# Kernel tuning notes

Hardware: AMD Instinct MI355X
Metric: run time of the kernel (lower is better)

## Reference

```python
import jax, jax.numpy as jnp
import numpy as np

D_MODEL = 256
D_INNER = 512          # expand * d_model
HEADDIM = 64
NHEADS = D_INNER // HEADDIM   # 8
NGROUPS = 1
D_STATE = 64
D_IN_PROJ = 2 * D_INNER + 2 * NGROUPS * D_STATE + NHEADS   # 1160
CONV_DIM = D_INNER + 2 * NGROUPS * D_STATE                  # 640
LN_EPS = 1e-5


def setup_inputs() -> dict:
    key = jax.random.key(0)
    ks = jax.random.split(key, 16)
    s = 0.02
    # dt_bias init as in torch code
    dt = jnp.exp(jax.random.uniform(ks[10], (NHEADS,)) * (np.log(0.1) - np.log(0.001)) + np.log(0.001))
    dt = jnp.clip(dt, 1e-4)
    dt_bias = dt + jnp.log(-jnp.expm1(-dt))
    A_log = jnp.log(jax.random.uniform(ks[11], (NHEADS,), minval=1.0, maxval=16.0))
    return {
        "u": jax.random.normal(ks[0], (4, 8192, D_MODEL), dtype=jnp.float32),
        "H": 64,
        "W": 128,
        "W_in": jax.random.normal(ks[1], (D_IN_PROJ, D_MODEL), dtype=jnp.float32) * s,
        "W_stereo": jax.random.normal(ks[2], (D_IN_PROJ, D_INNER), dtype=jnp.float32) * s,
        "conv_l_w": jax.random.normal(ks[3], (CONV_DIM, 1, 3, 3), dtype=jnp.float32) * 0.1,
        "conv_l_b": jax.random.normal(ks[4], (CONV_DIM,), dtype=jnp.float32) * 0.01,
        "conv_r_w": jax.random.normal(ks[5], (CONV_DIM, 1, 3, 3), dtype=jnp.float32) * 0.1,
        "conv_r_b": jax.random.normal(ks[6], (CONV_DIM,), dtype=jnp.float32) * 0.01,
        "conv_w": jax.random.normal(ks[7], (CONV_DIM, 1, 3, 3), dtype=jnp.float32) * 0.1,
        "conv_b": jax.random.normal(ks[8], (CONV_DIM,), dtype=jnp.float32) * 0.01,
        "dt_bias": dt_bias,
        "A_log": A_log,
        "D_l": jnp.ones((NHEADS,), dtype=jnp.float32),
        "D_r": jnp.ones((NHEADS,), dtype=jnp.float32),
        "D": jnp.ones((NHEADS,), dtype=jnp.float32),
        "ln_g": jnp.ones((D_INNER,), dtype=jnp.float32),
        "ln_b": jnp.zeros((D_INNER,), dtype=jnp.float32),
        "W_out": jax.random.normal(ks[9], (D_MODEL, D_INNER), dtype=jnp.float32) * s,
    }


def _dwconv(x, w, b):
    # x: (B, C, H, W); depthwise 3x3 conv, SAME padding ((d_conv-1)//2 = 1)
    y = jax.lax.conv_general_dilated(
        x, w, window_strides=(1, 1), padding='SAME',
        dimension_numbers=('NCHW', 'OIHW', 'NCHW'),
        feature_group_count=CONV_DIM)
    return y + b[None, :, None, None]


def _layernorm(x, g, b):
    mu = x.mean(-1, keepdims=True)
    var = x.var(-1, keepdims=True)
    return (x - mu) / jnp.sqrt(var + LN_EPS) * g + b


def _lin_attn(x, dt, A, Bm, Cm, Dp):
    # x: (b, l, d_inner), dt: (b, l, h), Bm/Cm: (b, l, d_state); ngroups == 1
    b, l, _ = x.shape
    xh = x.reshape(b, l, NHEADS, HEADDIM)              # V: (b, l, h, p)
    dA = -(dt[..., None] * A[None, None, :, None])     # ssd_positve_dA -> -dt*A, (b,l,h,1)
    KV = jnp.einsum('bls,blhp->bhsp', Bm, xh * dA)     # K^T @ V_scaled
    y = jnp.einsum('bls,bhsp->blhp', Cm, KV)           # Q @ KV
    y = y + xh * Dp[None, None, :, None]               # skip D
    return y.reshape(b, l, D_INNER)


def reference(u, H, W, W_in, W_stereo, conv_l_w, conv_l_b, conv_r_w, conv_r_b,
              conv_w, conv_b, dt_bias, A_log, D_l, D_r, D, ln_g, ln_b, W_out):
    batch, seqlen, _ = u.shape
    half = batch // 2
    silu = jax.nn.silu
    A = -jnp.exp(A_log)

    zxbcdt = u @ W_in.T                                             # (b, l, 1160)
    z, xBC, dt = jnp.split(zxbcdt, [D_INNER, D_INNER + CONV_DIM], axis=-1)
    dt = jax.nn.softplus(dt + dt_bias)                              # (b, l, h)

    xBC = xBC.reshape(batch, H, W, CONV_DIM).transpose(0, 3, 1, 2)  # NCHW
    xBC1 = silu(_dwconv(xBC[:half], conv_l_w, conv_l_b)).transpose(0, 2, 3, 1).reshape(half, H * W, CONV_DIM)
    xBC2 = silu(_dwconv(xBC[half:], conv_r_w, conv_r_b)).transpose(0, 2, 3, 1).reshape(half, H * W, CONV_DIM)

    x1, B1, C1 = jnp.split(xBC1, [D_INNER, D_INNER + NGROUPS * D_STATE], axis=-1)
    x2, B2, C2 = jnp.split(xBC2, [D_INNER, D_INNER + NGROUPS * D_STATE], axis=-1)
    dt1, dt2 = dt[:half], dt[half:]

    y1 = _layernorm(_lin_attn(x1, dt1, A, B1, C1, D_l), ln_g, ln_b)
    y2 = _layernorm(_lin_attn(x2, dt2, A, B2, C2, D_r), ln_g, ln_b)
    y = jnp.concatenate([y1, y2], axis=0) * z

    zxs = y @ W_stereo.T
    zs, xBCs, dts = jnp.split(zxs, [D_INNER, D_INNER + CONV_DIM], axis=-1)
    dts = jax.nn.softplus(dts + dt_bias)

    xBCs = xBCs.reshape(batch, H, W, CONV_DIM).transpose(0, 3, 1, 2)
    xBCs = silu(_dwconv(xBCs, conv_w, conv_b)).transpose(0, 2, 3, 1).reshape(batch, H * W, CONV_DIM)
    xs, Bs, Cs = jnp.split(xBCs, [D_INNER, D_INNER + NGROUPS * D_STATE], axis=-1)

    ys = _layernorm(_lin_attn(xs, dts, A, Bs, Cs, D), ln_g, ln_b) * zs
    return ys @ W_out.T
```

## Files before the change

### kernel.cpp

```cpp
#include <hip/hip_runtime.h>
#include <hip/hip_bf16.h>
#include <math.h>

#define NB    4
#define LSEQ  8192
#define HH    64
#define WW    128
#define DMODEL 256
#define DINNER 512
#define NH    8
#define DSTATE 64
#define DPROJ 1160
#define CONVD 640
#define MROWS (NB*LSEQ)
#define KVCH  32
#define CBLK  80

typedef unsigned short bf16_t;
typedef __attribute__((ext_vector_type(8))) unsigned short ushort8v;
typedef __attribute__((ext_vector_type(8))) short short8v;
typedef __attribute__((ext_vector_type(4))) float f32x4;

static __device__ __forceinline__ float bf2f(bf16_t u) {
    return __uint_as_float(((unsigned)u) << 16);
}
static __device__ __forceinline__ bf16_t f2bf(float f) {
    unsigned u = __float_as_uint(f);
    u += 0x7FFFu + ((u >> 16) & 1u);
    return (bf16_t)(u >> 16);
}

template <typename TC>
__global__ __launch_bounds__(512) void gemm_mfma_big(
    const bf16_t* __restrict__ A, int lda,
    const bf16_t* __restrict__ B, int ldb,
    TC* __restrict__ C, int ldc,
    int M, int N, int K)
{
    __shared__ __align__(16) bf16_t As[2][256 * 32];
    __shared__ __align__(16) bf16_t Bs[2][128 * 32];
    const int nwg = gridDim.x * gridDim.y;
    const int wg  = blockIdx.y * gridDim.x + blockIdx.x;
    const int swz = (wg & 7) * (nwg >> 3) + (wg >> 3);
    const int bx  = swz % gridDim.x;
    const int by  = swz / gridDim.x;

    const int tid = threadIdx.x;
    const int m0 = by * 256;
    const int n0 = bx * 128;
    const int w    = tid >> 6;
    const int lane = tid & 63;
    const int wrow = w >> 1;
    const int wcol = w & 1;
    const int fr = lane & 15;
    const int kq = lane >> 4;

    f32x4 acc[4][4];
    #pragma unroll
    for (int i = 0; i < 4; ++i)
        #pragma unroll
        for (int j = 0; j < 4; ++j) acc[i][j] = (f32x4){0.f, 0.f, 0.f, 0.f};

    int arow[2], acol[2];
    #pragma unroll
    for (int i = 0; i < 2; ++i) {
        const int L = i * 512 + tid;
        arow[i] = ((L >> 8) << 6) + (((L >> 6) & 3) << 4) + ((L >> 2) & 15);
        acol[i] = (L & 3) * 8;
    }
    const int Lb = tid;
    const int brow = ((Lb >> 8) << 6) + (((Lb >> 6) & 3) << 4) + ((Lb >> 2) & 15);
    const int bcol = (Lb & 3) * 8;

#define STAGE_BIG(buf, k0)                                                     \
    {                                                                          \
        _Pragma("unroll")                                                      \
        for (int i = 0; i < 2; ++i) {                                          \
            const size_t ga = (size_t)(m0 + arow[i]) * lda + (k0) + acol[i];   \
            __builtin_amdgcn_global_load_lds(                                  \
                (const __attribute__((address_space(1))) void*)(A + ga),       \
                (__attribute__((address_space(3))) void*)(&As[buf][(i * 512 + tid) * 8]), 16, 0, 0); \
        }                                                                      \
        const size_t gb = (size_t)(n0 + brow) * ldb + (k0) + bcol;             \
        __builtin_amdgcn_global_load_lds(                                      \
            (const __attribute__((address_space(1))) void*)(B + gb),           \
            (__attribute__((address_space(3))) void*)(&Bs[buf][tid * 8]), 16, 0, 0); \
    }

    const int nt = K >> 5;
    STAGE_BIG(0, 0);
    __syncthreads();

    const int abase = wrow * 2048 + (fr * 4 + kq) * 8;
    const int bbase = wcol * 2048 + (fr * 4 + kq) * 8;

    int cur = 0;
    for (int t = 0; t < nt; ++t) {
        if (t + 1 < nt) STAGE_BIG(cur ^ 1, (t + 1) * 32);

        short8v a_frag[4], b_frag[4];
        #pragma unroll
        for (int m = 0; m < 4; ++m)
            a_frag[m] = *(const short8v*)&As[cur][abase + m * 512];
        #pragma unroll
        for (int n = 0; n < 4; ++n)
            b_frag[n] = *(const short8v*)&Bs[cur][bbase + n * 512];
        #pragma unroll
        for (int m = 0; m < 4; ++m)
            #pragma unroll
            for (int n = 0; n < 4; ++n)
                acc[m][n] = __builtin_amdgcn_mfma_f32_16x16x32_bf16(
                    a_frag[m], b_frag[n], acc[m][n], 0, 0, 0);

        __syncthreads();
        cur ^= 1;
    }
#undef STAGE_BIG

    #pragma unroll
    for (int mi = 0; mi < 4; ++mi) {
        #pragma unroll
        for (int ni = 0; ni < 4; ++ni) {
            const int col = n0 + wcol * 64 + ni * 16 + fr;
            if (col < N) {
                #pragma unroll
                for (int q = 0; q < 4; ++q) {
                    const int row = m0 + wrow * 64 + mi * 16 + kq * 4 + q;
                    if constexpr (sizeof(TC) == 2)
                        C[(size_t)row * ldc + col] = f2bf(acc[mi][ni][q]);
                    else
                        C[(size_t)row * ldc + col] = acc[mi][ni][q];
                }
            }
        }
    }
}

template <typename TC>
__global__ __launch_bounds__(256) void gemm_mfma_bt(
    const bf16_t* __restrict__ A, int lda, size_t sAb,
    const bf16_t* __restrict__ B, int ldb, size_t sBb,
    TC* __restrict__ C, int ldc, size_t sCb,
    int M, int N, int K)
{
    __shared__ __align__(16) bf16_t As[128 * 32];
    __shared__ __align__(16) bf16_t Bs[128 * 32];
    const bf16_t* Ab = A + blockIdx.z * sAb;
    const bf16_t* Bb = B + blockIdx.z * sBb;
    TC*            Cb = C + blockIdx.z * sCb;
    const int tid = threadIdx.x;
    const int m0 = blockIdx.y * 128;
    const int n0 = blockIdx.x * 128;
    const int wid = tid >> 6;
    const int lane = tid & 63;
    const int wr = (wid >> 1) * 64;
    const int wc = (wid & 1) * 64;
    const int fr = lane & 15;
    const int fk = (lane >> 4) * 8;

    f32x4 acc[4][4];
    #pragma unroll
    for (int i = 0; i < 4; ++i)
        #pragma unroll
        for (int j = 0; j < 4; ++j) acc[i][j] = (f32x4){0.f, 0.f, 0.f, 0.f};

    const int srow = tid >> 2;
    const int scol = (tid & 3) * 8;
    const bf16_t* gA = Ab + (size_t)(m0 + srow) * lda + scol;
    const bf16_t* gB = Bb + (size_t)(n0 + srow) * ldb + scol;
    bf16_t* lA = As + tid * 8;
    bf16_t* lB = Bs + tid * 8;

    for (int k0 = 0; k0 < K; k0 += 32) {
        __builtin_amdgcn_global_load_lds(
            (const __attribute__((address_space(1))) void*)(gA + k0),
            (__attribute__((address_space(3))) void*)lA, 16, 0, 0);
        __builtin_amdgcn_global_load_lds(
            (const __attribute__((address_space(1))) void*)(gA + (size_t)64 * lda + k0),
            (__attribute__((address_space(3))) void*)(lA + 2048), 16, 0, 0);
        __builtin_amdgcn_global_load_lds(
            (const __attribute__((address_space(1))) void*)(gB + k0),
            (__attribute__((address_space(3))) void*)lB, 16, 0, 0);
        __builtin_amdgcn_global_load_lds(
            (const __attribute__((address_space(1))) void*)(gB + (size_t)64 * ldb + k0),
            (__attribute__((address_space(3))) void*)(lB + 2048), 16, 0, 0);
        __syncthreads();

        short8v a_frag[4], b_frag[4];
        #pragma unroll
        for (int m = 0; m < 4; ++m)
            a_frag[m] = *(const short8v*)&As[(wr + m * 16 + fr) * 32 + fk];
        #pragma unroll
        for (int n = 0; n < 4; ++n)
            b_frag[n] = *(const short8v*)&Bs[(wc + n * 16 + fr) * 32 + fk];
        #pragma unroll
        for (int m = 0; m < 4; ++m)
            #pragma unroll
            for (int n = 0; n < 4; ++n)
                acc[m][n] = __builtin_amdgcn_mfma_f32_16x16x32_bf16(
                    a_frag[m], b_frag[n], acc[m][n], 0, 0, 0);
        __syncthreads();
    }

    #pragma unroll
    for (int mi = 0; mi < 4; ++mi) {
        #pragma unroll
        for (int ni = 0; ni < 4; ++ni) {
            const int col = n0 + wc + ni * 16 + fr;
            if (col < N) {
                #pragma unroll
                for (int q = 0; q < 4; ++q) {
                    const int row = m0 + wr + mi * 16 + (lane >> 4) * 4 + q;
                    if constexpr (sizeof(TC) == 2)
                        Cb[(size_t)row * ldc + col] = f2bf(acc[mi][ni][q]);
                    else
                        Cb[(size_t)row * ldc + col] = acc[mi][ni][q];
                }
            }
        }
    }
}

__global__ __launch_bounds__(256) void cvt_bf16_kernel(
    const float* __restrict__ in, bf16_t* __restrict__ out, int n)
{
    const int base = (blockIdx.x * 256 + threadIdx.x) * 4;
    if (base >= n) return;
    float4 v = *(const float4*)&in[base];
    ushort4 o;
    o.x = f2bf(v.x); o.y = f2bf(v.y); o.z = f2bf(v.z); o.w = f2bf(v.w);
    *(ushort4*)&out[base] = o;
}

__global__ __launch_bounds__(256) void wpad_kernel(
    const float* __restrict__ W, bf16_t* __restrict__ Wp,
    int N, int Npad, int K)
{
    const int i = blockIdx.x * 256 + threadIdx.x;
    if (i >= Npad * K) return;
    const int r = i / K, k = i - r * K;
    Wp[i] = (r < N) ? f2bf(W[(size_t)r * K + k]) : (bf16_t)0;
}

__global__ __launch_bounds__(256) void dt_kernel(
    const bf16_t* __restrict__ zx, const float* __restrict__ dt_bias,
    float* __restrict__ dtbuf)
{
    const int idx = blockIdx.x * 256 + threadIdx.x;
    const int h = idx & 7;
    const int row = idx >> 3;
    const float v = bf2f(zx[(size_t)row * DPROJ + (DINNER + CONVD) + h]) + dt_bias[h];
    const float sp = (v > 0.f) ? (v + log1pf(expf(-v))) : log1pf(expf(v));
    dtbuf[idx] = sp;
}

__global__ __launch_bounds__(256) void conv_silu_kernel(
    const bf16_t* __restrict__ zx,
    const float* __restrict__ wA, const float* __restrict__ bA,
    const float* __restrict__ wB, const float* __restrict__ bB,
    bf16_t* __restrict__ out)
{
    const int idx = blockIdx.x * 256 + threadIdx.x;
    const int cb = idx % CBLK;
    const int pc = idx / CBLK;
    const int c0 = cb * 8;
    const int ww = pc & (WW - 1);
    const int h4 = (pc >> 7) & 15;
    const int b  = pc >> 11;
    const int hbase = h4 * 4;
    const float* wp = (b < 2) ? wA : wB;
    const float* bp = (b < 2) ? bA : bB;

    float w[72];
    const float4* wsrc = (const float4*)(wp + c0 * 9);
    #pragma unroll
    for (int i = 0; i < 18; ++i) ((float4*)w)[i] = wsrc[i];

    float acc[4][8];
    {
        float4 bv0 = *(const float4*)(bp + c0);
        float4 bv1 = *(const float4*)(bp + c0 + 4);
        #pragma unroll
        for (int o = 0; o < 4; ++o) {
            acc[o][0] = bv0.x; acc[o][1] = bv0.y; acc[o][2] = bv0.z; acc[o][3] = bv0.w;
            acc[o][4] = bv1.x; acc[o][5] = bv1.y; acc[o][6] = bv1.z; acc[o][7] = bv1.w;
        }
    }

    const bf16_t* base = zx + (size_t)b * LSEQ * DPROJ + DINNER + c0;
    #pragma unroll
    for (int ri = 0; ri < 6; ++ri) {
        const int hi = hbase + ri - 1;
        const bool hok = (unsigned)hi < (unsigned)HH;
        float cur[3][8];
        #pragma unroll
        for (int kj = 0; kj < 3; ++kj) {
            const int wi = ww + kj - 1;
            if (hok && (unsigned)wi < (unsigned)WW) {
                const ushort8v v = *(const ushort8v*)(base + (size_t)(hi * WW + wi) * DPROJ);
                #pragma unroll
                for (int q = 0; q < 8; ++q) cur[kj][q] = bf2f(v[q]);
            } else {
                #pragma unroll
                for (int q = 0; q < 8; ++q) cur[kj][q] = 0.f;
            }
        }
        #pragma unroll
        for (int o = 0; o < 4; ++o) {
            const int ki = ri - o;
            if (ki >= 0 && ki < 3) {
                #pragma unroll
                for (int kj = 0; kj < 3; ++kj)
                    #pragma unroll
                    for (int q = 0; q < 8; ++q)
                        acc[o][q] += cur[kj][q] * w[q * 9 + ki * 3 + kj];
            }
        }
    }

    #pragma unroll
    for (int o = 0; o < 4; ++o) {
        const int t = b * LSEQ + (hbase + o) * WW + ww;
        ushort8v ov;
        #pragma unroll
        for (int q = 0; q < 8; ++q) {
            const float s = acc[o][q] / (1.f + expf(-acc[o][q]));
            ov[q] = f2bf(s);
        }
        *(ushort8v*)(out + (size_t)t * CONVD + c0) = ov;
    }
}

__global__ __launch_bounds__(128) void kv_part_kernel(
    const bf16_t* __restrict__ xconv, const float* __restrict__ dtbuf,
    const float* __restrict__ A_log, float* __restrict__ KVp)
{
    const int h = blockIdx.y, b = blockIdx.z, chunk = blockIdx.x;
    const int tid = threadIdx.x;
    const int w = tid >> 6, lane = tid & 63;
    __shared__ float lds[2 * 4352];
    float* Bt = lds + w * 4352;
    float* Xt = Bt + 2176;
    const float eA = expf(A_log[h]);
    const int s4  = (lane & 15) * 4;
    const int p16 = (lane >> 4) * 16;
    const int r    = lane & 31;
    const int part = lane >> 5;

    float acc[4][16];
    #pragma unroll
    for (int i = 0; i < 4; ++i)
        #pragma unroll
        for (int j = 0; j < 16; ++j) acc[i][j] = 0.f;

    const int l0 = b * LSEQ + chunk * 256;

    for (int t = 0; t < 8; t += 2) {
        const int row = l0 + (t + w) * 32 + r;
        const bf16_t* src = xconv + (size_t)row * CONVD + (part ? h * 64 : DINNER);
        const float scale = part ? dtbuf[row * NH + h] * eA : 1.f;
        float* dst = part ? &Xt[r * 68] : &Bt[r * 68];
        #pragma unroll
        for (int j = 0; j < 8; ++j) {
            ushort8v v = *(const ushort8v*)(src + j * 8);
            f32x4 lo = {bf2f(v[0]) * scale, bf2f(v[1]) * scale,
                        bf2f(v[2]) * scale, bf2f(v[3]) * scale};
            f32x4 hi = {bf2f(v[4]) * scale, bf2f(v[5]) * scale,
                        bf2f(v[6]) * scale, bf2f(v[7]) * scale};
            *(f32x4*)&dst[j * 8]     = lo;
            *(f32x4*)&dst[j * 8 + 4] = hi;
        }
        __syncthreads();
        #pragma unroll 4
        for (int rr = 0; rr < 32; ++rr) {
            const f32x4 bv = *(const f32x4*)&Bt[rr * 68 + s4];
            #pragma unroll
            for (int q = 0; q < 4; ++q) {
                const f32x4 xv = *(const f32x4*)&Xt[rr * 68 + p16 + q * 4];
                #pragma unroll
                for (int si = 0; si < 4; ++si)
                    #pragma unroll
                    for (int k = 0; k < 4; ++k)
                        acc[si][q * 4 + k] += bv[si] * xv[k];
            }
        }
        __syncthreads();
    }

    if (w == 0) {
        #pragma unroll
        for (int si = 0; si < 4; ++si)
            #pragma unroll
            for (int q = 0; q < 4; ++q)
                *(f32x4*)&lds[(s4 + si) * 68 + p16 + q * 4] =
                    (f32x4){acc[si][q*4], acc[si][q*4+1], acc[si][q*4+2], acc[si][q*4+3]};
    }
    __syncthreads();
    if (w == 1) {
        float* dst = KVp + ((size_t)chunk * (NB * NH) + (b * NH + h)) * 4096;
        #pragma unroll
        for (int si = 0; si < 4; ++si)
            #pragma unroll
            for (int q = 0; q < 4; ++q) {
                const f32x4 o = *(const f32x4*)&lds[(s4 + si) * 68 + p16 + q * 4];
                f32x4 v = {acc[si][q*4] + o[0], acc[si][q*4+1] + o[1],
                           acc[si][q*4+2] + o[2], acc[si][q*4+3] + o[3]};
                *(f32x4*)&dst[(s4 + si) * 64 + p16 + q * 4] = v;
            }
    }
}

__global__ __launch_bounds__(256) void kv_reduce_T_kernel(
    const float* __restrict__ KVp, bf16_t* __restrict__ KVT)
{
    const int idx = blockIdx.x * 256 + threadIdx.x;
    float s = 0.f;
    #pragma unroll
    for (int c = 0; c < KVCH; ++c) s += KVp[(size_t)c * 131072 + idx];
    const int bh = idx >> 12;
    const int ss = (idx >> 6) & 63;
    const int p  = idx & 63;
    KVT[((size_t)(bh * 64 + p)) * 64 + ss] = f2bf(s);
}

__global__ __launch_bounds__(256) void ln_gate_kernel(
    const bf16_t* __restrict__ Yattn, const bf16_t* __restrict__ xconv,
    const bf16_t* __restrict__ zx,
    const float* __restrict__ DA, const float* __restrict__ DB,
    const float* __restrict__ ln_g, const float* __restrict__ ln_b,
    bf16_t* __restrict__ ybuf)
{
    const int w = threadIdx.x >> 6, lane = threadIdx.x & 63;
    const int c0 = lane * 8;
    const int h = lane >> 3;
    float g[8], be[8];
    *(float4*)&g[0]  = *(const float4*)&ln_g[c0];
    *(float4*)&g[4]  = *(const float4*)&ln_g[c0 + 4];
    *(float4*)&be[0] = *(const float4*)&ln_b[c0];
    *(float4*)&be[4] = *(const float4*)&ln_b[c0 + 4];
    const int row0 = (blockIdx.x * 4 + w) * 4;

    for (int i = 0; i < 4; ++i) {
        const int row = row0 + i;
        const int b = row >> 13;
        const float Dv = (b < 2) ? DA[h] : DB[h];
        ushort8v yv = *(const ushort8v*)(Yattn + (size_t)row * DINNER + c0);
        ushort8v xv = *(const ushort8v*)(xconv + (size_t)row * CONVD + c0);
        float y[8];
        float s1 = 0.f, s2 = 0.f;
        #pragma unroll
        for (int q = 0; q < 8; ++q) {
            y[q] = bf2f(yv[q]) + bf2f(xv[q]) * Dv;
            s1 += y[q]; s2 += y[q] * y[q];
        }
        #pragma unroll
        for (int off = 32; off > 0; off >>= 1) {
            s1 += __shfl_xor(s1, off, 64);
            s2 += __shfl_xor(s2, off, 64);
        }
        const float mu = s1 * (1.f / 512.f);
        const float var = s2 * (1.f / 512.f) - mu * mu;
        const float rstd = rsqrtf(var + 1e-5f);
        ushort8v zv = *(const ushort8v*)(zx + (size_t)row * DPROJ + c0);
        ushort8v o;
        #pragma unroll
        for (int q = 0; q < 8; ++q)
            o[q] = f2bf(((y[q] - mu) * rstd * g[q] + be[q]) * bf2f(zv[q]));
        *(ushort8v*)(ybuf + (size_t)row * DINNER + c0) = o;
    }
}

extern "C" void kernel_launch(void* const* d_in, const int* in_sizes, int n_in,
                              void* d_out, int out_size, void* d_ws, size_t ws_size,
                              hipStream_t stream)
{
    const float* u        = (const float*)d_in[0];
    const float* W_in     = (const float*)d_in[3];
    const float* W_st     = (const float*)d_in[4];
    const float* conv_l_w = (const float*)d_in[5];
    const float* conv_l_b = (const float*)d_in[6];
    const float* conv_r_w = (const float*)d_in[7];
    const float* conv_r_b = (const float*)d_in[8];
    const float* conv_w   = (const float*)d_in[9];
    const float* conv_b   = (const float*)d_in[10];
    const float* dt_bias  = (const float*)d_in[11];
    const float* A_log    = (const float*)d_in[12];
    const float* D_l      = (const float*)d_in[13];
    const float* D_r      = (const float*)d_in[14];
    const float* Dp       = (const float*)d_in[15];
    const float* ln_g     = (const float*)d_in[16];
    const float* ln_b     = (const float*)d_in[17];
    const float* W_out    = (const float*)d_in[18];
    float* out = (float*)d_out;

    char* ws = (char*)d_ws;
    const size_t ZX_B    = (size_t)MROWS * DPROJ * 2;
    const size_t XCONV_B = (size_t)MROWS * CONVD * 2;
    const size_t YBUF_B  = (size_t)MROWS * DINNER * 2;
    const size_t DT_B    = (size_t)MROWS * NH * 4;
    const size_t KVT_B   = (size_t)NB * DINNER * 64 * 2;
    const size_t UBF_B   = (size_t)MROWS * DMODEL * 2;
    const size_t WIN_B   = (size_t)1280 * DMODEL * 2;
    const size_t WST_B   = (size_t)1280 * DINNER * 2;
    const size_t WOUT_B  = (size_t)256 * DINNER * 2;
    bf16_t* zx    = (bf16_t*)(ws);
    bf16_t* xconv = (bf16_t*)(ws + ZX_B);
    bf16_t* ybuf  = (bf16_t*)(ws + ZX_B + XCONV_B);
    float*  dtbuf = (float*) (ws + ZX_B + XCONV_B + YBUF_B);
    bf16_t* KVT   = (bf16_t*)(ws + ZX_B + XCONV_B + YBUF_B + DT_B);
    bf16_t* ubf   = (bf16_t*)(ws + ZX_B + XCONV_B + YBUF_B + DT_B + KVT_B);
    float*  KVp   = (float*) (ws + ZX_B + XCONV_B + YBUF_B + DT_B + KVT_B);
    bf16_t* WinP  = (bf16_t*)(ws + ZX_B + XCONV_B + YBUF_B + DT_B + KVT_B + UBF_B);
    bf16_t* WstP  = (bf16_t*)(ws + ZX_B + XCONV_B + YBUF_B + DT_B + KVT_B + UBF_B + WIN_B);
    bf16_t* WoutP = (bf16_t*)(ws + ZX_B + XCONV_B + YBUF_B + DT_B + KVT_B + UBF_B + WIN_B + WST_B);
    bf16_t* Yattn = (bf16_t*)(ws + ZX_B + XCONV_B + YBUF_B + DT_B + KVT_B + UBF_B + WIN_B + WST_B + WOUT_B);

    const dim3 gemmGridP(10, MROWS / 256);
    const dim3 gemmGridO(2,  MROWS / 256);
    const dim3 ymmGrid(4, LSEQ / 128, NB);
    const dim3 kvGrid(KVCH, NH, NB);
    const int convGrid = (MROWS / 4) * CBLK / 256;
    const int lnGrid = MROWS / 16;

    cvt_bf16_kernel<<<(MROWS * DMODEL / 4 + 255) / 256, 256, 0, stream>>>(u, ubf, MROWS * DMODEL);
    wpad_kernel<<<(1280 * DMODEL + 255) / 256, 256, 0, stream>>>(W_in, WinP, DPROJ, 1280, DMODEL);
    wpad_kernel<<<(1280 * DINNER + 255) / 256, 256, 0, stream>>>(W_st, WstP, DPROJ, 1280, DINNER);
    wpad_kernel<<<(256 * DINNER + 255) / 256, 256, 0, stream>>>(W_out, WoutP, DMODEL, 256, DINNER);

    gemm_mfma_big<bf16_t><<<gemmGridP, 512, 0, stream>>>(
        ubf, DMODEL, WinP, DMODEL, zx, DPROJ, MROWS, DPROJ, DMODEL);
    dt_kernel<<<(MROWS * NH) / 256, 256, 0, stream>>>(zx, dt_bias, dtbuf);
    conv_silu_kernel<<<convGrid, 256, 0, stream>>>(
        zx, conv_l_w, conv_l_b, conv_r_w, conv_r_b, xconv);
    kv_part_kernel<<<kvGrid, 128, 0, stream>>>(xconv, dtbuf, A_log, KVp);
    kv_reduce_T_kernel<<<131072 / 256, 256, 0, stream>>>(KVp, KVT);
    gemm_mfma_bt<bf16_t><<<ymmGrid, 256, 0, stream>>>(
        xconv + DINNER + DSTATE, CONVD, (size_t)LSEQ * CONVD,
        KVT, 64, (size_t)DINNER * 64,
        Yattn, DINNER, (size_t)LSEQ * DINNER, LSEQ, DINNER, 64);
    ln_gate_kernel<<<lnGrid, 256, 0, stream>>>(
        Yattn, xconv, zx, D_l, D_r, ln_g, ln_b, ybuf);

    gemm_mfma_big<bf16_t><<<gemmGridP, 512, 0, stream>>>(
        ybuf, DINNER, WstP, DINNER, zx, DPROJ, MROWS, DPROJ, DINNER);
    dt_kernel<<<(MROWS * NH) / 256, 256, 0, stream>>>(zx, dt_bias, dtbuf);
    conv_silu_kernel<<<convGrid, 256, 0, stream>>>(
        zx, conv_w, conv_b, conv_w, conv_b, xconv);
    kv_part_kernel<<<kvGrid, 128, 0, stream>>>(xconv, dtbuf, A_log, KVp);
    kv_reduce_T_kernel<<<131072 / 256, 256, 0, stream>>>(KVp, KVT);
    gemm_mfma_bt<bf16_t><<<ymmGrid, 256, 0, stream>>>(
        xconv + DINNER + DSTATE, CONVD, (size_t)LSEQ * CONVD,
        KVT, 64, (size_t)DINNER * 64,
        Yattn, DINNER, (size_t)LSEQ * DINNER, LSEQ, DINNER, 64);
    ln_gate_kernel<<<lnGrid, 256, 0, stream>>>(
        Yattn, xconv, zx, Dp, Dp, ln_g, ln_b, ybuf);

    gemm_mfma_big<float><<<gemmGridO, 512, 0, stream>>>(
        ybuf, DINNER, WoutP, DINNER, out, DMODEL, MROWS, DMODEL, DINNER);
}
```

Baseline: 387.2 us.

## Fuse softplus dt into kv_part, widen conv tile, switch output GEMM kernel

Removes the separate dt_kernel and computes softplus(dt + bias) inline inside kv_part_kernel, dropping a launch and the dtbuf round trip. The depthwise conv kernel now computes two adjacent output columns per thread, so neighbouring input columns are loaded once and shared, and its grid is halved. The final output projection switches from gemm_mfma_big with 512 threads to gemm_mfma_bt with 256 threads on a 128-row grid. These are three independent changes, and the conv change raises register pressure.

```diff
diff --git a/kernel.cpp b/kernel.cpp
--- a/kernel.cpp
+++ b/kernel.cpp
@@ -242,18 +242,6 @@
     Wp[i] = (r < N) ? f2bf(W[(size_t)r * K + k]) : (bf16_t)0;
 }
 
-__global__ __launch_bounds__(256) void dt_kernel(
-    const bf16_t* __restrict__ zx, const float* __restrict__ dt_bias,
-    float* __restrict__ dtbuf)
-{
-    const int idx = blockIdx.x * 256 + threadIdx.x;
-    const int h = idx & 7;
-    const int row = idx >> 3;
-    const float v = bf2f(zx[(size_t)row * DPROJ + (DINNER + CONVD) + h]) + dt_bias[h];
-    const float sp = (v > 0.f) ? (v + log1pf(expf(-v))) : log1pf(expf(v));
-    dtbuf[idx] = sp;
-}
-
 __global__ __launch_bounds__(256) void conv_silu_kernel(
     const bf16_t* __restrict__ zx,
     const float* __restrict__ wA, const float* __restrict__ bA,
@@ -264,10 +252,11 @@
     const int cb = idx % CBLK;
     const int pc = idx / CBLK;
     const int c0 = cb * 8;
-    const int ww = pc & (WW - 1);
-    const int h4 = (pc >> 7) & 15;
-    const int b  = pc >> 11;
+    const int w2 = pc & 63;
+    const int h4 = (pc >> 6) & 15;
+    const int b  = pc >> 10;
     const int hbase = h4 * 4;
+    const int wbase = w2 * 2;
     const float* wp = (b < 2) ? wA : wB;
     const float* bp = (b < 2) ? bA : bB;
 
@@ -276,15 +265,19 @@
     #pragma unroll
     for (int i = 0; i < 18; ++i) ((float4*)w)[i] = wsrc[i];
 
-    float acc[4][8];
+    float acc[4][2][8];
     {
         float4 bv0 = *(const float4*)(bp + c0);
         float4 bv1 = *(const float4*)(bp + c0 + 4);
         #pragma unroll
-        for (int o = 0; o < 4; ++o) {
-            acc[o][0] = bv0.x; acc[o][1] = bv0.y; acc[o][2] = bv0.z; acc[o][3] = bv0.w;
-            acc[o][4] = bv1.x; acc[o][5] = bv1.y; acc[o][6] = bv1.z; acc[o][7] = bv1.w;
-        }
+        for (int o = 0; o < 4; ++o)
+            #pragma unroll
+            for (int ow = 0; ow < 2; ++ow) {
+                acc[o][ow][0] = bv0.x; acc[o][ow][1] = bv0.y;
+                acc[o][ow][2] = bv0.z; acc[o][ow][3] = bv0.w;
+                acc[o][ow][4] = bv1.x; acc[o][ow][5] = bv1.y;
+                acc[o][ow][6] = bv1.z; acc[o][ow][7] = bv1.w;
+            }
     }
 
     const bf16_t* base = zx + (size_t)b * LSEQ * DPROJ + DINNER + c0;
@@ -292,10 +285,10 @@
     for (int ri = 0; ri < 6; ++ri) {
         const int hi = hbase + ri - 1;
         const bool hok = (unsigned)hi < (unsigned)HH;
-        float cur[3][8];
-        #pragma unroll
-        for (int kj = 0; kj < 3; ++kj) {
-            const int wi = ww + kj - 1;
+        float cur[4][8];
+        #pragma unroll
+        for (int kj = 0; kj < 4; ++kj) {
+            const int wi = wbase + kj - 1;
             if (hok && (unsigned)wi < (unsigned)WW) {
                 const ushort8v v = *(const ushort8v*)(base + (size_t)(hi * WW + wi) * DPROJ);
                 #pragma unroll
@@ -310,29 +303,34 @@
             const int ki = ri - o;
             if (ki >= 0 && ki < 3) {
                 #pragma unroll
-                for (int kj = 0; kj < 3; ++kj)
+                for (int ow = 0; ow < 2; ++ow)
                     #pragma unroll
-                    for (int q = 0; q < 8; ++q)
-                        acc[o][q] += cur[kj][q] * w[q * 9 + ki * 3 + kj];
-            }
-        }
-    }
-
-    #pragma unroll
-    for (int o = 0; o < 4; ++o) {
-        const int t = b * LSEQ + (hbase + o) * WW + ww;
-        ushort8v ov;
-        #pragma unroll
-        for (int q = 0; q < 8; ++q) {
-            const float s = acc[o][q] / (1.f + expf(-acc[o][q]));
-            ov[q] = f2bf(s);
-        }
-        *(ushort8v*)(out + (size_t)t * CONVD + c0) = ov;
-    }
+                    for (int tc = 0; tc < 3; ++tc)
+                        #pragma unroll
+                        for (int q = 0; q < 8; ++q)
+                            acc[o][ow][q] += cur[ow + tc][q] * w[q * 9 + ki * 3 + tc];
+            }
+        }
+    }
+
+    #pragma unroll
+    for (int o = 0; o < 4; ++o)
+        #pragma unroll
+        for (int ow = 0; ow < 2; ++ow) {
+            const int t = b * LSEQ + (hbase + o) * WW + (wbase + ow);
+            ushort8v ov;
+            #pragma unroll
+            for (int q = 0; q < 8; ++q) {
+                const float s = acc[o][ow][q] / (1.f + expf(-acc[o][ow][q]));
+                ov[q] = f2bf(s);
+            }
+            *(ushort8v*)(out + (size_t)t * CONVD + c0) = ov;
+        }
 }
 
 __global__ __launch_bounds__(128) void kv_part_kernel(
-    const bf16_t* __restrict__ xconv, const float* __restrict__ dtbuf,
+    const bf16_t* __restrict__ xconv, const bf16_t* __restrict__ zx,
+    const float* __restrict__ dt_bias,
     const float* __restrict__ A_log, float* __restrict__ KVp)
 {
     const int h = blockIdx.y, b = blockIdx.z, chunk = blockIdx.x;
@@ -342,6 +340,7 @@
     float* Bt = lds + w * 4352;
     float* Xt = Bt + 2176;
     const float eA = expf(A_log[h]);
+    const float dtb = dt_bias[h];
     const int s4  = (lane & 15) * 4;
     const int p16 = (lane >> 4) * 16;
     const int r    = lane & 31;
@@ -358,7 +357,12 @@
     for (int t = 0; t < 8; t += 2) {
         const int row = l0 + (t + w) * 32 + r;
         const bf16_t* src = xconv + (size_t)row * CONVD + (part ? h * 64 : DINNER);
-        const float scale = part ? dtbuf[row * NH + h] * eA : 1.f;
+        float scale = 1.f;
+        if (part) {
+            const float v = bf2f(zx[(size_t)row * DPROJ + (DINNER + CONVD) + h]) + dtb;
+            const float sp = (v > 0.f) ? (v + log1pf(expf(-v))) : log1pf(expf(v));
+            scale = sp * eA;
+        }
         float* dst = part ? &Xt[r * 68] : &Bt[r * 68];
         #pragma unroll
         for (int j = 0; j < 8; ++j) {
@@ -506,7 +510,6 @@
     bf16_t* zx    = (bf16_t*)(ws);
     bf16_t* xconv = (bf16_t*)(ws + ZX_B);
     bf16_t* ybuf  = (bf16_t*)(ws + ZX_B + XCONV_B);
-    float*  dtbuf = (float*) (ws + ZX_B + XCONV_B + YBUF_B);
     bf16_t* KVT   = (bf16_t*)(ws + ZX_B + XCONV_B + YBUF_B + DT_B);
     bf16_t* ubf   = (bf16_t*)(ws + ZX_B + XCONV_B + YBUF_B + DT_B + KVT_B);
     float*  KVp   = (float*) (ws + ZX_B + XCONV_B + YBUF_B + DT_B + KVT_B);
@@ -516,10 +519,10 @@
     bf16_t* Yattn = (bf16_t*)(ws + ZX_B + XCONV_B + YBUF_B + DT_B + KVT_B + UBF_B + WIN_B + WST_B + WOUT_B);
 
     const dim3 gemmGridP(10, MROWS / 256);
-    const dim3 gemmGridO(2,  MROWS / 256);
+    const dim3 gemmGridO(2,  MROWS / 128, 1);
     const dim3 ymmGrid(4, LSEQ / 128, NB);
     const dim3 kvGrid(KVCH, NH, NB);
-    const int convGrid = (MROWS / 4) * CBLK / 256;
+    const int convGrid = (MROWS / 8) * CBLK / 256;
     const int lnGrid = MROWS / 16;
 
     cvt_bf16_kernel<<<(MROWS * DMODEL / 4 + 255) / 256, 256, 0, stream>>>(u, ubf, MROWS * DMODEL);
@@ -529,10 +532,9 @@
 
     gemm_mfma_big<bf16_t><<<gemmGridP, 512, 0, stream>>>(
         ubf, DMODEL, WinP, DMODEL, zx, DPROJ, MROWS, DPROJ, DMODEL);
-    dt_kernel<<<(MROWS * NH) / 256, 256, 0, stream>>>(zx, dt_bias, dtbuf);
     conv_silu_kernel<<<convGrid, 256, 0, stream>>>(
         zx, conv_l_w, conv_l_b, conv_r_w, conv_r_b, xconv);
-    kv_part_kernel<<<kvGrid, 128, 0, stream>>>(xconv, dtbuf, A_log, KVp);
+    kv_part_kernel<<<kvGrid, 128, 0, stream>>>(xconv, zx, dt_bias, A_log, KVp);
     kv_reduce_T_kernel<<<131072 / 256, 256, 0, stream>>>(KVp, KVT);
     gemm_mfma_bt<bf16_t><<<ymmGrid, 256, 0, stream>>>(
         xconv + DINNER + DSTATE, CONVD, (size_t)LSEQ * CONVD,
@@ -543,10 +545,9 @@
 
     gemm_mfma_big<bf16_t><<<gemmGridP, 512, 0, stream>>>(
         ybuf, DINNER, WstP, DINNER, zx, DPROJ, MROWS, DPROJ, DINNER);
-    dt_kernel<<<(MROWS * NH) / 256, 256, 0, stream>>>(zx, dt_bias, dtbuf);
     conv_silu_kernel<<<convGrid, 256, 0, stream>>>(
         zx, conv_w, conv_b, conv_w, conv_b, xconv);
-    kv_part_kernel<<<kvGrid, 128, 0, stream>>>(xconv, dtbuf, A_log, KVp);
+    kv_part_kernel<<<kvGrid, 128, 0, stream>>>(xconv, zx, dt_bias, A_log, KVp);
     kv_reduce_T_kernel<<<131072 / 256, 256, 0, stream>>>(KVp, KVT);
     gemm_mfma_bt<bf16_t><<<ymmGrid, 256, 0, stream>>>(
         xconv + DINNER + DSTATE, CONVD, (size_t)LSEQ * CONVD,
@@ -555,6 +556,6 @@
     ln_gate_kernel<<<lnGrid, 256, 0, stream>>>(
         Yattn, xconv, zx, Dp, Dp, ln_g, ln_b, ybuf);
 
-    gemm_mfma_big<float><<<gemmGridO, 512, 0, stream>>>(
-        ybuf, DINNER, WoutP, DINNER, out, DMODEL, MROWS, DMODEL, DINNER);
-}
+    gemm_mfma_bt<float><<<gemmGridO, 256, 0, stream>>>(
+        ybuf, DINNER, 0, WoutP, DINNER, 0, out, DMODEL, 0, MROWS, DMODEL, DINNER);
+}
```

Result: slower. 409.7 us (+5.8%).
